# Optimization experiments

Measured on AMD Instinct MI355X. Metric: run time of the kernel, lower is better.

## Reference

```python
import jax, jax.numpy as jnp
import numpy as np

B, N, C = 2, 2048, 768
H = 16
D = C // H  # head_dim = 48
SCALE = 1.0 / float(np.sqrt(D))


def setup_inputs() -> dict:
    key = jax.random.key(0)
    ks = jax.random.split(key, 5)
    x = jax.random.normal(ks[0], (B, N, C), dtype=jnp.float32)
    # torch nn.Linear weights are [out, in]; apply as x @ W.T
    qkv_w = jax.random.normal(ks[1], (3 * C, C), dtype=jnp.float32) * 0.02
    qkv_b = jax.random.normal(ks[2], (3 * C,), dtype=jnp.float32) * 0.02
    proj_w = jax.random.normal(ks[3], (C, C), dtype=jnp.float32) * 0.02
    proj_b = jax.random.normal(ks[4], (C,), dtype=jnp.float32) * 0.02
    return {"x": x, "qkv_w": qkv_w, "qkv_b": qkv_b, "proj_w": proj_w, "proj_b": proj_b}


def reference(x, qkv_w, qkv_b, proj_w, proj_b):
    # qkv: (B, N, 3C) -> (3, B, H, N, D)
    qkv = x @ qkv_w.T + qkv_b
    qkv = qkv.reshape(B, N, 3, H, D).transpose(2, 0, 3, 1, 4)
    q, k, v = qkv[0], qkv[1], qkv[2]
    # manual attention: full (B, H, N, N) score matrix, as in the original
    attn = jnp.einsum('bhqd,bhkd->bhqk', q, k) * SCALE
    attn = jax.nn.softmax(attn, axis=-1)
    # attn_drop with p=0.0 (eval / deterministic) is identity
    y = jnp.einsum('bhqk,bhkd->bhqd', attn, v)
    y = y.transpose(0, 2, 1, 3).reshape(B, N, C)
    return y @ proj_w.T + proj_b
```

## Files before the change

kernel.cpp:

```cpp
#include <hip/hip_runtime.h>

typedef short v8s __attribute__((ext_vector_type(8)));
typedef short v4s __attribute__((ext_vector_type(4)));
typedef float v4f __attribute__((ext_vector_type(4)));
typedef unsigned uint2v __attribute__((ext_vector_type(2)));
typedef unsigned short u16;

#define NSEQ 2048
#define CDIM 768
#define NH   16
#define DH   48
#define DP   64
#define MROWS 4096
#define N3C  2304
#define BH   32

#if __has_builtin(__builtin_amdgcn_exp2f)
#define EXP2(x) __builtin_amdgcn_exp2f(x)
#else
#define EXP2(x) exp2f(x)
#endif
#if __has_builtin(__builtin_amdgcn_rcpf)
#define RCP(x) __builtin_amdgcn_rcpf(x)
#else
#define RCP(x) (1.0f/(x))
#endif

__device__ __forceinline__ u16 f2bf(float f){
  unsigned u = __float_as_uint(f);
  u += 0x7FFFu + ((u>>16)&1u);
  return (u16)(u>>16);
}
__device__ __forceinline__ unsigned pkbf(float a, float b){
  unsigned x = __float_as_uint(a), y = __float_as_uint(b);
  x += 0x7FFFu + ((x>>16)&1u);
  y += 0x7FFFu + ((y>>16)&1u);
  return (x>>16) | (y & 0xFFFF0000u);
}

__device__ __forceinline__ void load_lds16(const u16* g, u16* l){
  __builtin_amdgcn_global_load_lds((const __attribute__((address_space(1))) void*)g,
                                   (__attribute__((address_space(3))) void*)l, 16, 0, 0);
}

#define XN8  (MROWS*CDIM/8)
#define WN8  (N3C*CDIM/8)
#define PN8  (CDIM*CDIM/8)
#define CONVB ((XN8+WN8+PN8)/256)
__global__ __launch_bounds__(256) void prep(const float* __restrict__ x, const float* __restrict__ w,
                                            const float* __restrict__ pw, u16* __restrict__ dst,
                                            u16* __restrict__ q, u16* __restrict__ k, u16* __restrict__ v){
  int bid = blockIdx.x;
  if (bid < CONVB){
    int i = bid*256 + threadIdx.x;
    const float* src;
    if (i < XN8)            src = x  + (size_t)i*8;
    else if (i < XN8+WN8)   src = w  + (size_t)(i - XN8)*8;
    else                    src = pw + (size_t)(i - XN8 - WN8)*8;
    v4f f0 = ((const v4f*)src)[0];
    v4f f1 = ((const v4f*)src)[1];
    v8s o;
#pragma unroll
    for (int j = 0; j < 4; j++) ((u16*)&o)[j]   = f2bf(f0[j]);
#pragma unroll
    for (int j = 0; j < 4; j++) ((u16*)&o)[4+j] = f2bf(f1[j]);
    ((v8s*)dst)[i] = o;
  } else {
    int idx = (bid - CONVB)*256 + threadIdx.x;
    v8s z = (v8s){0,0,0,0,0,0,0,0};
    int r = idx >> 1, half = idx & 1;
    *(v8s*)(q + (size_t)r*DP + DH + half*8) = z;
    *(v8s*)(k + (size_t)r*DP + DH + half*8) = z;
  }
}

__global__ __launch_bounds__(256) void qkv_gemm(const u16* __restrict__ x, const u16* __restrict__ w,
                                                const float* __restrict__ bias,
                                                u16* __restrict__ q, u16* __restrict__ k, u16* __restrict__ v){
  __shared__ __align__(16) u16 As[128*32];
  __shared__ __align__(16) u16 Bs[128*32];
  const int wave = threadIdx.x >> 6;
  const int lane = threadIdx.x & 63;
  const int l15  = lane & 15;
  const int quad = lane >> 4;
  const int wm = wave & 1, wn = wave >> 1;
  const int m0 = blockIdx.x*128, n0 = blockIdx.y*128;

  const int srow = lane >> 2;
  const int sg   = (lane & 3) ^ ((lane >> 3) & 3);
  const int sgoff = sg*8;

  v4f acc[4][4];
#pragma unroll
  for (int i = 0; i < 4; i++)
#pragma unroll
    for (int j = 0; j < 4; j++) acc[i][j] = (v4f){0.f,0.f,0.f,0.f};

  const int sig = (l15 >> 1) & 3;

  for (int kt = 0; kt < CDIM/32; kt++){
    const int k0 = kt*32;
    __syncthreads();
#pragma unroll
    for (int j = 0; j < 2; j++){
      int c = wave*2 + j;
      int r = c*16 + srow;
      load_lds16(x + (size_t)(m0 + r)*CDIM + k0 + sgoff, &As[c*512]);
      load_lds16(w + (size_t)(n0 + r)*CDIM + k0 + sgoff, &Bs[c*512]);
    }
    __syncthreads();

    v8s af[4], bf[4];
#pragma unroll
    for (int t = 0; t < 4; t++){
      int ra = wm*64 + t*16 + l15;
      af[t] = *(const v8s*)(&As[ra*32 + ((quad ^ sig)<<3)]);
      int rb = wn*64 + t*16 + l15;
      bf[t] = *(const v8s*)(&Bs[rb*32 + ((quad ^ sig)<<3)]);
    }
#pragma unroll
    for (int ti = 0; ti < 4; ti++)
#pragma unroll
      for (int tj = 0; tj < 4; tj++)
        acc[ti][tj] = __builtin_amdgcn_mfma_f32_16x16x32_bf16(af[ti], bf[tj], acc[ti][tj], 0, 0, 0);
  }

  const float QS = 0.2082540589f;
#pragma unroll
  for (int tj = 0; tj < 4; tj++){
    const int c = n0 + wn*64 + tj*16 + l15;
    const float bv = bias[c];
    const int t = c / CDIM;
    const int rem = c - t*CDIM;
    const int h = rem / DH;
    const int d = rem - h*DH;
#pragma unroll
    for (int ti = 0; ti < 4; ti++){
#pragma unroll
      for (int r = 0; r < 4; r++){
        int m = m0 + wm*64 + ti*16 + quad*4 + r;
        int b_ = m >> 11;
        int n  = m & (NSEQ-1);
        float val = acc[ti][tj][r] + bv;
        if (t == 0) val *= QS;
        u16 o  = f2bf(val);
        int bhn = b_*NH + h;
        if (t == 0)      q[((size_t)bhn*NSEQ + n)*DP + d] = o;
        else if (t == 1) k[((size_t)bhn*NSEQ + n)*DP + d] = o;
        else             v[((size_t)bhn*DP + d)*NSEQ + n] = o;
      }
    }
  }
}

__global__ __launch_bounds__(256) void attn(const u16* __restrict__ q, const u16* __restrict__ k,
                                            const u16* __restrict__ v,
                                            float* __restrict__ oacc, float* __restrict__ lacc){
  __shared__ __align__(16) u16 Kl[64*64];
  __shared__ __align__(16) u16 Vl[48*64];
  __shared__ __align__(16) u16 Pl[4*2*1024];
  const int bh = blockIdx.x;
  const int qt = blockIdx.y;
  const int sp = blockIdx.z;
  const int wave = threadIdx.x >> 6;
  const int lane = threadIdx.x & 63;
  const int l15  = lane & 15;
  const int quad = lane >> 4;
  const int lo3  = l15 & 7;
  const u16* qb = q + (size_t)bh*NSEQ*DP;
  const u16* kb = k + (size_t)bh*NSEQ*DP;
  const u16* vb = v + (size_t)bh*DP*NSEQ;
  const int qm = qt*128 + wave*32;

  v8s qf[2][2];
#pragma unroll
  for (int si = 0; si < 2; si++)
#pragma unroll
    for (int ks = 0; ks < 2; ks++)
      qf[si][ks] = *(const v8s*)(qb + (size_t)(qm + si*16 + l15)*DP + ks*32 + quad*8);

  const short one = (short)0x3F80;
  const v8s vones = (l15 == 0) ? (v8s){one,one,one,one,one,one,one,one}
                               : (v8s){0,0,0,0,0,0,0,0};

  v4f o[2][4];
#pragma unroll
  for (int si = 0; si < 2; si++)
#pragma unroll
    for (int i = 0; i < 4; i++) o[si][i] = (v4f){0.f,0.f,0.f,0.f};

  const int sr  = lane >> 3;
  const int soff = ((lane & 7) ^ (sr & 7)) * 8;
  u16* Plw = Pl + wave*2048;

  for (int kt = sp*16; kt < sp*16 + 16; kt++){
    __syncthreads();
    {
#pragma unroll
      for (int p = 0; p < 2; p++){
        int row = p*32 + wave*8 + sr;
        load_lds16(kb + ((size_t)(kt*64 + row))*DP + soff, &Kl[(p*32 + wave*8)*64]);
      }
      {
        int row = wave*8 + sr;
        load_lds16(vb + (size_t)row*NSEQ + kt*64 + soff, &Vl[(wave*8)*64]);
      }
      if (wave < 2){
        int row = 32 + wave*8 + sr;
        load_lds16(vb + (size_t)row*NSEQ + kt*64 + soff, &Vl[(32 + wave*8)*64]);
      }
    }
    __syncthreads();

#pragma unroll
    for (int si = 0; si < 2; si++){
      v4f s[4];
#pragma unroll
      for (int nt = 0; nt < 4; nt++){
        s[nt] = (v4f){0.f,0.f,0.f,0.f};
#pragma unroll
        for (int ks = 0; ks < 2; ks++){
          int rrow = nt*16 + l15;
          v8s kf = *(const v8s*)(&Kl[rrow*64 + (((ks*4+quad) ^ lo3)<<3)]);
          s[nt] = __builtin_amdgcn_mfma_f32_16x16x32_bf16(kf, qf[si][ks], s[nt], 0, 0, 0);
        }
      }
#pragma unroll
      for (int nt = 0; nt < 4; nt++){
        uint2v pw;
        pw.x = pkbf(EXP2(s[nt][0]), EXP2(s[nt][1]));
        pw.y = pkbf(EXP2(s[nt][2]), EXP2(s[nt][3]));
        int g = nt*2 + (quad>>1);
        *(uint2v*)(&Plw[si*1024 + l15*64 + ((g ^ lo3)<<3) + (quad&1)*4]) = pw;
      }
    }

    v8s pa[2][2];
#pragma unroll
    for (int si = 0; si < 2; si++)
#pragma unroll
      for (int ks = 0; ks < 2; ks++){
        int ga = ks*4 + quad;
        pa[si][ks] = *(const v8s*)(&Plw[si*1024 + l15*64 + ((ga ^ lo3)<<3)]);
      }
#pragma unroll
    for (int dt = 0; dt < 3; dt++){
#pragma unroll
      for (int ks = 0; ks < 2; ks++){
        int row = dt*16 + l15;
        v8s vf = *(const v8s*)(&Vl[row*64 + (((ks*4+quad) ^ lo3)<<3)]);
        o[0][dt] = __builtin_amdgcn_mfma_f32_16x16x32_bf16(pa[0][ks], vf, o[0][dt], 0, 0, 0);
        o[1][dt] = __builtin_amdgcn_mfma_f32_16x16x32_bf16(pa[1][ks], vf, o[1][dt], 0, 0, 0);
      }
    }
#pragma unroll
    for (int ks = 0; ks < 2; ks++){
      o[0][3] = __builtin_amdgcn_mfma_f32_16x16x32_bf16(pa[0][ks], vones, o[0][3], 0, 0, 0);
      o[1][3] = __builtin_amdgcn_mfma_f32_16x16x32_bf16(pa[1][ks], vones, o[1][3], 0, 0, 0);
    }
  }

  const int b_ = bh / NH, h = bh % NH;
  float* oa = oacc + (size_t)sp*MROWS*CDIM;
  float* la = lacc + (size_t)sp*MROWS*NH;
#pragma unroll
  for (int si = 0; si < 2; si++){
#pragma unroll
    for (int r = 0; r < 4; r++){
      int rowg = b_*NSEQ + qm + si*16 + quad*4 + r;
#pragma unroll
      for (int dt = 0; dt < 3; dt++)
        oa[(size_t)rowg*CDIM + h*DH + dt*16 + l15] = o[si][dt][r];
      if (l15 == 0) la[rowg*NH + h] = o[si][3][r];
    }
  }
}

__global__ __launch_bounds__(256) void finalize(const float* __restrict__ oacc,
                                                const float* __restrict__ lacc,
                                                u16* __restrict__ y){
  int i = blockIdx.x*256 + threadIdx.x;
  int rowg = i / 192, c4 = i - rowg*192;
  int c = c4*4, h = c / DH;
  float l = lacc[rowg*NH + h] + lacc[MROWS*NH + rowg*NH + h];
  float inv = RCP(l);
  v4f a = *(const v4f*)(oacc + (size_t)rowg*CDIM + c);
  v4f b = *(const v4f*)(oacc + (size_t)MROWS*CDIM + (size_t)rowg*CDIM + c);
  v4s o4;
#pragma unroll
  for (int j = 0; j < 4; j++) o4[j] = (short)f2bf((a[j] + b[j])*inv);
  *(v4s*)(y + (size_t)rowg*CDIM + c) = o4;
}

__global__ __launch_bounds__(256) void proj_gemm(const u16* __restrict__ y, const u16* __restrict__ w,
                                                 const float* __restrict__ bias, float* __restrict__ out){
  __shared__ __align__(16) u16 As[64*32];
  __shared__ __align__(16) u16 Bs[128*32];
  const int wave = threadIdx.x >> 6;
  const int lane = threadIdx.x & 63;
  const int l15  = lane & 15;
  const int quad = lane >> 4;
  const int wm = wave & 1, wn = wave >> 1;
  const int m0 = blockIdx.x*64, n0 = blockIdx.y*128;

  const int srow = lane >> 2;
  const int sg   = (lane & 3) ^ ((lane >> 3) & 3);
  const int sgoff = sg*8;

  v4f acc[2][4];
#pragma unroll
  for (int i = 0; i < 2; i++)
#pragma unroll
    for (int j = 0; j < 4; j++) acc[i][j] = (v4f){0.f,0.f,0.f,0.f};

  const int sig = (l15 >> 1) & 3;

  for (int kt = 0; kt < CDIM/32; kt++){
    const int k0 = kt*32;
    __syncthreads();
    {
      int rA = wave*16 + srow;
      load_lds16(y + (size_t)(m0 + rA)*CDIM + k0 + sgoff, &As[wave*512]);
#pragma unroll
      for (int j = 0; j < 2; j++){
        int c = wave*2 + j;
        int rB = c*16 + srow;
        load_lds16(w + (size_t)(n0 + rB)*CDIM + k0 + sgoff, &Bs[c*512]);
      }
    }
    __syncthreads();

    v8s af[2], bf[4];
#pragma unroll
    for (int t = 0; t < 2; t++){
      int ra = wm*32 + t*16 + l15;
      af[t] = *(const v8s*)(&As[ra*32 + ((quad ^ sig)<<3)]);
    }
#pragma unroll
    for (int t = 0; t < 4; t++){
      int rb = wn*64 + t*16 + l15;
      bf[t] = *(const v8s*)(&Bs[rb*32 + ((quad ^ sig)<<3)]);
    }
#pragma unroll
    for (int ti = 0; ti < 2; ti++)
#pragma unroll
      for (int tj = 0; tj < 4; tj++)
        acc[ti][tj] = __builtin_amdgcn_mfma_f32_16x16x32_bf16(af[ti], bf[tj], acc[ti][tj], 0, 0, 0);
  }

#pragma unroll
  for (int tj = 0; tj < 4; tj++){
    const int c = n0 + wn*64 + tj*16 + l15;
    const float bv = bias[c];
#pragma unroll
    for (int ti = 0; ti < 2; ti++){
#pragma unroll
      for (int r = 0; r < 4; r++){
        int m = m0 + wm*32 + ti*16 + quad*4 + r;
        out[(size_t)m*CDIM + c] = acc[ti][tj][r] + bv;
      }
    }
  }
}

extern "C" void kernel_launch(void* const* d_in, const int* in_sizes, int n_in,
                              void* d_out, int out_size, void* d_ws, size_t ws_size,
                              hipStream_t stream){
  const float* x      = (const float*)d_in[0];
  const float* qkv_w  = (const float*)d_in[1];
  const float* qkv_b  = (const float*)d_in[2];
  const float* proj_w = (const float*)d_in[3];
  const float* proj_b = (const float*)d_in[4];
  float* out = (float*)d_out;

  u16* xb  = (u16*)d_ws;
  u16* wb  = xb  + (size_t)MROWS*CDIM;
  u16* pwb = wb  + (size_t)N3C*CDIM;
  u16* q   = pwb + (size_t)CDIM*CDIM;
  u16* k   = q + (size_t)BH*NSEQ*DP;
  u16* v   = k + (size_t)BH*NSEQ*DP;
  float* oacc = (float*)(v + (size_t)BH*NSEQ*DP);
  float* lacc = oacc + (size_t)2*MROWS*CDIM;
  u16* y = xb;

  prep<<<dim3(CONVB + 512), dim3(256), 0, stream>>>(x, qkv_w, proj_w, xb, q, k, v);
  qkv_gemm<<<dim3(MROWS/128, N3C/128), dim3(256), 0, stream>>>(xb, wb, qkv_b, q, k, v);
  attn<<<dim3(BH, NSEQ/128, 2), dim3(256), 0, stream>>>(q, k, v, oacc, lacc);
  finalize<<<dim3(MROWS*192/256), dim3(256), 0, stream>>>(oacc, lacc, y);
  proj_gemm<<<dim3(MROWS/64, CDIM/128), dim3(256), 0, stream>>>(y, pwb, proj_b, out);
}
```

Measured before the change: 174.4 us.

## Shrink GEMM tiles, use hardware bf16 pack, and interleave QK MFMAs in attention

The QKV GEMM tile drops from 128x128 to 64x128 and the projection GEMM tile from 64x128 to 64x64, doubling the block count of each to fill more compute units. In attention, the P bf16 packing uses the hardware cvt_pk_bf16_f32 builtin when available, and the QK^T loop is restructured so each K fragment is loaded once and reused across both query sub-tiles. An unused v parameter is dropped from prep. Smaller tiles lower per-block data reuse and add global/LDS traffic in exchange for better occupancy and load balance.

```diff
diff --git a/kernel.cpp b/kernel.cpp
--- a/kernel.cpp
+++ b/kernel.cpp
@@ -31,12 +31,21 @@
   u += 0x7FFFu + ((u>>16)&1u);
   return (u16)(u>>16);
 }
+
+#if __has_builtin(__builtin_amdgcn_cvt_pk_bf16_f32)
+typedef __bf16 bf16x2_t __attribute__((ext_vector_type(2)));
+__device__ __forceinline__ unsigned pkbf(float a, float b){
+  bf16x2_t r = __builtin_amdgcn_cvt_pk_bf16_f32(a, b);
+  return __builtin_bit_cast(unsigned, r);
+}
+#else
 __device__ __forceinline__ unsigned pkbf(float a, float b){
   unsigned x = __float_as_uint(a), y = __float_as_uint(b);
   x += 0x7FFFu + ((x>>16)&1u);
   y += 0x7FFFu + ((y>>16)&1u);
   return (x>>16) | (y & 0xFFFF0000u);
 }
+#endif
 
 __device__ __forceinline__ void load_lds16(const u16* g, u16* l){
   __builtin_amdgcn_global_load_lds((const __attribute__((address_space(1))) void*)g,
@@ -49,7 +58,7 @@
 #define CONVB ((XN8+WN8+PN8)/256)
 __global__ __launch_bounds__(256) void prep(const float* __restrict__ x, const float* __restrict__ w,
                                             const float* __restrict__ pw, u16* __restrict__ dst,
-                                            u16* __restrict__ q, u16* __restrict__ k, u16* __restrict__ v){
+                                            u16* __restrict__ q, u16* __restrict__ k){
   int bid = blockIdx.x;
   if (bid < CONVB){
     int i = bid*256 + threadIdx.x;
@@ -77,22 +86,22 @@
 __global__ __launch_bounds__(256) void qkv_gemm(const u16* __restrict__ x, const u16* __restrict__ w,
                                                 const float* __restrict__ bias,
                                                 u16* __restrict__ q, u16* __restrict__ k, u16* __restrict__ v){
-  __shared__ __align__(16) u16 As[128*32];
+  __shared__ __align__(16) u16 As[64*32];
   __shared__ __align__(16) u16 Bs[128*32];
   const int wave = threadIdx.x >> 6;
   const int lane = threadIdx.x & 63;
   const int l15  = lane & 15;
   const int quad = lane >> 4;
   const int wm = wave & 1, wn = wave >> 1;
-  const int m0 = blockIdx.x*128, n0 = blockIdx.y*128;
+  const int m0 = blockIdx.x*64, n0 = blockIdx.y*128;
 
   const int srow = lane >> 2;
   const int sg   = (lane & 3) ^ ((lane >> 3) & 3);
   const int sgoff = sg*8;
 
-  v4f acc[4][4];
-#pragma unroll
-  for (int i = 0; i < 4; i++)
+  v4f acc[2][4];
+#pragma unroll
+  for (int i = 0; i < 2; i++)
 #pragma unroll
     for (int j = 0; j < 4; j++) acc[i][j] = (v4f){0.f,0.f,0.f,0.f};
 
@@ -101,25 +110,31 @@
   for (int kt = 0; kt < CDIM/32; kt++){
     const int k0 = kt*32;
     __syncthreads();
-#pragma unroll
-    for (int j = 0; j < 2; j++){
-      int c = wave*2 + j;
-      int r = c*16 + srow;
-      load_lds16(x + (size_t)(m0 + r)*CDIM + k0 + sgoff, &As[c*512]);
-      load_lds16(w + (size_t)(n0 + r)*CDIM + k0 + sgoff, &Bs[c*512]);
-    }
-    __syncthreads();
-
-    v8s af[4], bf[4];
+    {
+      int rA = wave*16 + srow;
+      load_lds16(x + (size_t)(m0 + rA)*CDIM + k0 + sgoff, &As[wave*512]);
+#pragma unroll
+      for (int j = 0; j < 2; j++){
+        int c = wave*2 + j;
+        int rB = c*16 + srow;
+        load_lds16(w + (size_t)(n0 + rB)*CDIM + k0 + sgoff, &Bs[c*512]);
+      }
+    }
+    __syncthreads();
+
+    v8s af[2], bf[4];
+#pragma unroll
+    for (int t = 0; t < 2; t++){
+      int ra = wm*32 + t*16 + l15;
+      af[t] = *(const v8s*)(&As[ra*32 + ((quad ^ sig)<<3)]);
+    }
 #pragma unroll
     for (int t = 0; t < 4; t++){
-      int ra = wm*64 + t*16 + l15;
-      af[t] = *(const v8s*)(&As[ra*32 + ((quad ^ sig)<<3)]);
       int rb = wn*64 + t*16 + l15;
       bf[t] = *(const v8s*)(&Bs[rb*32 + ((quad ^ sig)<<3)]);
     }
 #pragma unroll
-    for (int ti = 0; ti < 4; ti++)
+    for (int ti = 0; ti < 2; ti++)
 #pragma unroll
       for (int tj = 0; tj < 4; tj++)
         acc[ti][tj] = __builtin_amdgcn_mfma_f32_16x16x32_bf16(af[ti], bf[tj], acc[ti][tj], 0, 0, 0);
@@ -135,10 +150,10 @@
     const int h = rem / DH;
     const int d = rem - h*DH;
 #pragma unroll
-    for (int ti = 0; ti < 4; ti++){
+    for (int ti = 0; ti < 2; ti++){
 #pragma unroll
       for (int r = 0; r < 4; r++){
-        int m = m0 + wm*64 + ti*16 + quad*4 + r;
+        int m = m0 + wm*32 + ti*16 + quad*4 + r;
         int b_ = m >> 11;
         int n  = m & (NSEQ-1);
         float val = acc[ti][tj][r] + bv;
@@ -212,28 +227,28 @@
     }
     __syncthreads();
 
-#pragma unroll
-    for (int si = 0; si < 2; si++){
-      v4f s[4];
-#pragma unroll
-      for (int nt = 0; nt < 4; nt++){
-        s[nt] = (v4f){0.f,0.f,0.f,0.f};
-#pragma unroll
-        for (int ks = 0; ks < 2; ks++){
-          int rrow = nt*16 + l15;
-          v8s kf = *(const v8s*)(&Kl[rrow*64 + (((ks*4+quad) ^ lo3)<<3)]);
-          s[nt] = __builtin_amdgcn_mfma_f32_16x16x32_bf16(kf, qf[si][ks], s[nt], 0, 0, 0);
-        }
-      }
+    v4f s[2][4];
+#pragma unroll
+    for (int nt = 0; nt < 4; nt++){
+      int rrow = nt*16 + l15;
+      v8s kf0 = *(const v8s*)(&Kl[rrow*64 + ((quad ^ lo3)<<3)]);
+      v8s kf1 = *(const v8s*)(&Kl[rrow*64 + (((4+quad) ^ lo3)<<3)]);
+      s[0][nt] = __builtin_amdgcn_mfma_f32_16x16x32_bf16(kf0, qf[0][0], (v4f){0.f,0.f,0.f,0.f}, 0, 0, 0);
+      s[0][nt] = __builtin_amdgcn_mfma_f32_16x16x32_bf16(kf1, qf[0][1], s[0][nt], 0, 0, 0);
+      s[1][nt] = __builtin_amdgcn_mfma_f32_16x16x32_bf16(kf0, qf[1][0], (v4f){0.f,0.f,0.f,0.f}, 0, 0, 0);
+      s[1][nt] = __builtin_amdgcn_mfma_f32_16x16x32_bf16(kf1, qf[1][1], s[1][nt], 0, 0, 0);
+    }
+
+#pragma unroll
+    for (int si = 0; si < 2; si++)
 #pragma unroll
       for (int nt = 0; nt < 4; nt++){
         uint2v pw;
-        pw.x = pkbf(EXP2(s[nt][0]), EXP2(s[nt][1]));
-        pw.y = pkbf(EXP2(s[nt][2]), EXP2(s[nt][3]));
+        pw.x = pkbf(EXP2(s[si][nt][0]), EXP2(s[si][nt][1]));
+        pw.y = pkbf(EXP2(s[si][nt][2]), EXP2(s[si][nt][3]));
         int g = nt*2 + (quad>>1);
         *(uint2v*)(&Plw[si*1024 + l15*64 + ((g ^ lo3)<<3) + (quad&1)*4]) = pw;
       }
-    }
 
     v8s pa[2][2];
 #pragma unroll
@@ -295,23 +310,23 @@
 __global__ __launch_bounds__(256) void proj_gemm(const u16* __restrict__ y, const u16* __restrict__ w,
                                                  const float* __restrict__ bias, float* __restrict__ out){
   __shared__ __align__(16) u16 As[64*32];
-  __shared__ __align__(16) u16 Bs[128*32];
+  __shared__ __align__(16) u16 Bs[64*32];
   const int wave = threadIdx.x >> 6;
   const int lane = threadIdx.x & 63;
   const int l15  = lane & 15;
   const int quad = lane >> 4;
   const int wm = wave & 1, wn = wave >> 1;
-  const int m0 = blockIdx.x*64, n0 = blockIdx.y*128;
+  const int m0 = blockIdx.x*64, n0 = blockIdx.y*64;
 
   const int srow = lane >> 2;
   const int sg   = (lane & 3) ^ ((lane >> 3) & 3);
   const int sgoff = sg*8;
 
-  v4f acc[2][4];
+  v4f acc[2][2];
 #pragma unroll
   for (int i = 0; i < 2; i++)
 #pragma unroll
-    for (int j = 0; j < 4; j++) acc[i][j] = (v4f){0.f,0.f,0.f,0.f};
+    for (int j = 0; j < 2; j++) acc[i][j] = (v4f){0.f,0.f,0.f,0.f};
 
   const int sig = (l15 >> 1) & 3;
 
@@ -321,36 +336,29 @@
     {
       int rA = wave*16 + srow;
       load_lds16(y + (size_t)(m0 + rA)*CDIM + k0 + sgoff, &As[wave*512]);
-#pragma unroll
-      for (int j = 0; j < 2; j++){
-        int c = wave*2 + j;
-        int rB = c*16 + srow;
-        load_lds16(w + (size_t)(n0 + rB)*CDIM + k0 + sgoff, &Bs[c*512]);
-      }
-    }
-    __syncthreads();
-
-    v8s af[2], bf[4];
+      int rB = wave*16 + srow;
+      load_lds16(w + (size_t)(n0 + rB)*CDIM + k0 + sgoff, &Bs[wave*512]);
+    }
+    __syncthreads();
+
+    v8s af[2], bf[2];
 #pragma unroll
     for (int t = 0; t < 2; t++){
       int ra = wm*32 + t*16 + l15;
       af[t] = *(const v8s*)(&As[ra*32 + ((quad ^ sig)<<3)]);
-    }
-#pragma unroll
-    for (int t = 0; t < 4; t++){
-      int rb = wn*64 + t*16 + l15;
+      int rb = wn*32 + t*16 + l15;
       bf[t] = *(const v8s*)(&Bs[rb*32 + ((quad ^ sig)<<3)]);
     }
 #pragma unroll
     for (int ti = 0; ti < 2; ti++)
 #pragma unroll
-      for (int tj = 0; tj < 4; tj++)
+      for (int tj = 0; tj < 2; tj++)
         acc[ti][tj] = __builtin_amdgcn_mfma_f32_16x16x32_bf16(af[ti], bf[tj], acc[ti][tj], 0, 0, 0);
   }
 
 #pragma unroll
-  for (int tj = 0; tj < 4; tj++){
-    const int c = n0 + wn*64 + tj*16 + l15;
+  for (int tj = 0; tj < 2; tj++){
+    const int c = n0 + wn*32 + tj*16 + l15;
     const float bv = bias[c];
 #pragma unroll
     for (int ti = 0; ti < 2; ti++){
@@ -383,9 +391,9 @@
   float* lacc = oacc + (size_t)2*MROWS*CDIM;
   u16* y = xb;
 
-  prep<<<dim3(CONVB + 512), dim3(256), 0, stream>>>(x, qkv_w, proj_w, xb, q, k, v);
-  qkv_gemm<<<dim3(MROWS/128, N3C/128), dim3(256), 0, stream>>>(xb, wb, qkv_b, q, k, v);
+  prep<<<dim3(CONVB + 512), dim3(256), 0, stream>>>(x, qkv_w, proj_w, xb, q, k);
+  qkv_gemm<<<dim3(MROWS/64, N3C/128), dim3(256), 0, stream>>>(xb, wb, qkv_b, q, k, v);
   attn<<<dim3(BH, NSEQ/128, 2), dim3(256), 0, stream>>>(q, k, v, oacc, lacc);
   finalize<<<dim3(MROWS*192/256), dim3(256), 0, stream>>>(oacc, lacc, y);
-  proj_gemm<<<dim3(MROWS/64, CDIM/128), dim3(256), 0, stream>>>(y, pwb, proj_b, out);
-}
+  proj_gemm<<<dim3(MROWS/64, CDIM/64), dim3(256), 0, stream>>>(y, pwb, proj_b, out);
+}
```

After: 175.9 us. About the same (+0.9%).
